# Performance work log

Measured on AMD Instinct MI355X. Metric: run time of the kernel, lower is better.

The kernel has to match this reference:

```python
import jax, jax.numpy as jnp
import numpy as np

N_NODES, N_EDGES, N_GRAPHS, D = 32768, 49152, 1024, 64


def setup_inputs() -> dict:
    key = jax.random.key(0)
    ks = jax.random.split(key, 24)
    p = lambda k, shape, s=0.1: jax.random.normal(k, shape, dtype=jnp.float32) * s
    return dict(
        x=jax.random.normal(ks[0], (N_NODES, 14), dtype=jnp.float32),
        edge_index=jax.random.randint(ks[1], (2, N_EDGES), 0, N_NODES),
        edge_attr=jax.random.uniform(ks[2], (N_EDGES, 4), dtype=jnp.float32),
        batch=jnp.sort(jax.random.randint(ks[3], (N_NODES,), 0, N_GRAPHS)),
        lin0_W=p(ks[4], (D, 14)), lin0_b=p(ks[5], (D,)),
        e1_W=p(ks[6], (128, 4)), e1_b=p(ks[7], (128,)),
        e2_W=p(ks[8], (D * D, 128), 0.02), e2_b=p(ks[9], (D * D,), 0.02),
        root_W=p(ks[10], (D, D)), conv_b=p(ks[11], (D,)),
        gru_Wih=p(ks[12], (3 * D, D)), gru_Whh=p(ks[13], (3 * D, D)),
        gru_bih=p(ks[14], (3 * D,)), gru_bhh=p(ks[15], (3 * D,)),
        lstm_Wih=p(ks[16], (4 * D, 2 * D)), lstm_Whh=p(ks[17], (4 * D, D)),
        lstm_bih=p(ks[18], (4 * D,)), lstm_bhh=p(ks[19], (4 * D,)),
        fc1_W=p(ks[20], (128, 2 * D)), fc1_b=p(ks[21], (128,)),
        fc2_W=p(ks[22], (1, 128)), fc2_b=p(ks[23], (1,)),
    )


def reference(x, edge_index, edge_attr, batch,
              lin0_W, lin0_b, e1_W, e1_b, e2_W, e2_b, root_W, conv_b,
              gru_Wih, gru_Whh, gru_bih, gru_bhh,
              lstm_Wih, lstm_Whh, lstm_bih, lstm_bhh,
              fc1_W, fc1_b, fc2_W, fc2_b):
    N, B = x.shape[0], N_GRAPHS
    src, dst = edge_index[0], edge_index[1]

    out = jax.nn.relu(x @ lin0_W.T + lin0_b)            # [N, D]
    h = out                                             # GRU hidden (num_layers=1)

    # Edge-conditioned weights: edge_attr is constant across the 3 iterations,
    # so compute the edge MLP once (identical math to re-running it).
    W = jax.nn.relu(edge_attr @ e1_W.T + e1_b) @ e2_W.T + e2_b
    W = W.reshape(-1, D, D)                             # [E, D, D]
    cnt = jnp.maximum(
        jax.ops.segment_sum(jnp.ones((src.shape[0],), x.dtype), dst, num_segments=N), 1.0)

    for _ in range(3):
        # NNConv (aggr='mean'): gather -> per-edge matmul -> scatter-mean -> root + bias
        msg = jnp.einsum('ei,eio->eo', out[src], W)     # [E, D]
        agg = jax.ops.segment_sum(msg, dst, num_segments=N) / cnt[:, None]
        m = jax.nn.relu(agg + out @ root_W + conv_b)
        # GRU cell (seq_len=1)
        gi = m @ gru_Wih.T + gru_bih
        gh = h @ gru_Whh.T + gru_bhh
        ir, iz, inn = jnp.split(gi, 3, -1)
        hr, hz, hn = jnp.split(gh, 3, -1)
        r = jax.nn.sigmoid(ir + hr)
        z = jax.nn.sigmoid(iz + hz)
        n = jnp.tanh(inn + r * hn)
        h = (1.0 - z) * n + z * h
        out = h

    # Set2Set pooling, 3 processing steps, LSTM(2D -> D)
    q_star = jnp.zeros((B, 2 * D), x.dtype)
    hl = jnp.zeros((B, D), x.dtype)
    cl = jnp.zeros((B, D), x.dtype)
    for _ in range(3):
        g = q_star @ lstm_Wih.T + lstm_bih + hl @ lstm_Whh.T + lstm_bhh
        i_, f_, g_, o_ = jnp.split(g, 4, -1)
        cl = jax.nn.sigmoid(f_) * cl + jax.nn.sigmoid(i_) * jnp.tanh(g_)
        hl = jax.nn.sigmoid(o_) * jnp.tanh(cl)
        q = hl                                          # [B, D]
        e = jnp.sum(out * q[batch], -1)                 # [N]
        mx = jax.ops.segment_max(e, batch, num_segments=B)
        ex = jnp.exp(e - mx[batch])
        den = jax.ops.segment_sum(ex, batch, num_segments=B)
        a = ex / den[batch]                             # segment softmax
        r_read = jax.ops.segment_sum(a[:, None] * out, batch, num_segments=B)
        q_star = jnp.concatenate([q, r_read], -1)       # [B, 2D]

    hid = jax.nn.relu(q_star @ fc1_W.T + fc1_b)
    return hid @ fc2_W.T + fc2_b                        # [B, 1]
```

## Files before the change

kernel.cpp:

```cpp
#include <hip/hip_runtime.h>
#include <math.h>

#define NN_ 32768
#define NE_ 49152
#define NG_ 1024

typedef short bh8 __attribute__((ext_vector_type(8)));
typedef float f32x4 __attribute__((ext_vector_type(4)));

__device__ __forceinline__ unsigned short f2bfu(float f) {
    union { float f; unsigned int i; } x; x.f = f;
    unsigned int u = x.i;
    u += 0x7FFFu + ((u >> 16) & 1u);
    return (unsigned short)(u >> 16);
}
__device__ __forceinline__ float sigm(float x) { return 1.f / (1.f + expf(-x)); }

__global__ void MPNN_78632261256134_kernel() {}

__global__ void k_zero(float* p, int n) {
    int i = blockIdx.x * 256 + threadIdx.x;
    if (i < n) p[i] = 0.f;
}

__global__ void k_init(float* cnt, float* qstar) {
    int i = blockIdx.x * 256 + threadIdx.x;
    if (i < NN_) cnt[i] = 0.f;
    else if (i < NN_ + NG_ * 256) qstar[i - NN_] = 0.f;
}

__global__ void k_lin0(const float* x, const float* W, const float* b, float* node) {
    int g = blockIdx.x * 256 + threadIdx.x;
    int n = g >> 6, d = g & 63;
    const float* xr = x + n * 14;
    const float* wr = W + d * 14;
    float acc = b[d];
    for (int i = 0; i < 14; i++) acc += xr[i] * wr[i];
    node[g] = fmaxf(acc, 0.f);
}

__global__ void k_cnt(const int* dst, float* cnt) {
    int e = blockIdx.x * 256 + threadIdx.x;
    if (e < NE_) atomicAdd(&cnt[dst[e]], 1.0f);
}

__global__ void k_tw(const float* gWih, const float* gWhh, float* WihT, float* WhhT,
                     const float* lWih, const float* lWhh, float* WihT2, float* WhhT2) {
    int t = blockIdx.x * 256 + threadIdx.x;
    if (t < 12288) {
        int gr = t >> 6, i = t & 63; WihT[i * 192 + gr] = gWih[t];
    } else if (t < 24576) {
        int u = t - 12288; int gr = u >> 6, i = u & 63; WhhT[i * 192 + gr] = gWhh[u];
    } else if (t < 57344) {
        int u = t - 24576; int r = u >> 7, c = u & 127; WihT2[c * 256 + r] = lWih[u];
    } else if (t < 73728) {
        int u = t - 57344; int r = u >> 6, c = u & 63; WhhT2[c * 256 + r] = lWhh[u];
    }
}

__global__ void k_bhat3(const float* e2W, unsigned short* Bhat3) {
    int idx = blockIdx.x * 256 + threadIdx.x;
    if (idx >= 64 * 4 * 4 * 64 * 8) return;
    int j = idx & 7, lane = (idx >> 3) & 63, t = (idx >> 9) & 3, w = (idx >> 11) & 3, s = idx >> 13;
    int row = s * 64 + w * 16 + (lane & 15);
    int k = t * 32 + (lane >> 4) * 8 + j;
    Bhat3[idx] = f2bfu(e2W[row * 128 + k]);
}

__global__ __launch_bounds__(256) void k_he(const float* __restrict__ ea,
                                            const float* __restrict__ e1W,
                                            const float* __restrict__ e1b,
                                            unsigned short* __restrict__ Hhat) {
    int tid = threadIdx.x;
    int lane = tid & 63, sub = tid >> 6;
    int gi = blockIdx.x * 4 + sub;
    int etile = gi >> 2, t = gi & 3;
    int e = etile * 16 + (lane & 15), quad = lane >> 4;
    const float* ar = ea + (size_t)e * 4;
    float a0 = ar[0], a1 = ar[1], a2 = ar[2], a3 = ar[3];
    union { unsigned short u[8]; uint4 q; } o;
#pragma unroll
    for (int j = 0; j < 8; j++) {
        int c = t * 32 + quad * 8 + j;
        const float* wr = e1W + c * 4;
        float h = e1b[c] + a0 * wr[0] + a1 * wr[1] + a2 * wr[2] + a3 * wr[3];
        o.u[j] = f2bfu(fmaxf(h, 0.f));
    }
    *(uint4*)(Hhat + (size_t)gi * 512 + lane * 8) = o.q;
}

#define PS(S) (((S) + soff) & 63)

#define LDB(B, S) {                                                                       \
        const unsigned short* _p = Bhat3 + (size_t)PS(S) * 8192 + w * 2048 + lane * 8;    \
        (B)[0] = *(const bh8*)(const void*)(_p);                                          \
        (B)[1] = *(const bh8*)(const void*)(_p + 512);                                    \
        (B)[2] = *(const bh8*)(const void*)(_p + 1024);                                   \
        (B)[3] = *(const bh8*)(const void*)(_p + 1536); }

#define MFMA16(ACC, B) {                                                                  \
        _Pragma("unroll")                                                                 \
        for (int t_ = 0; t_ < 4; t_++) {                                                  \
            _Pragma("unroll")                                                             \
            for (int mt_ = 0; mt_ < 4; mt_++)                                             \
                (ACC)[mt_] = __builtin_amdgcn_mfma_f32_16x16x32_bf16(                     \
                    af[mt_][t_], (B)[t_], (t_ == 0) ? z4 : (ACC)[mt_], 0, 0, 0);          \
        } }

#define CONSUME(ACC, S) {                                                                 \
        int sp_ = PS(S);                                                                  \
        float bb_ = ebs[sp_ * 64 + w * 16 + mrow];                                        \
        _Pragma("unroll")                                                                 \
        for (int mt_ = 0; mt_ < 4; mt_++) {                                               \
            f32x4 xv_ = *(const f32x4*)(const void*)(xs + sp_ * 68 + mt_ * 16 + quad * 4);\
            _Pragma("unroll")                                                             \
            for (int r_ = 0; r_ < 4; r_++)                                                \
                msg[mt_][r_] += xv_[r_] * ((ACC)[mt_][r_] + bb_);                         \
        } }

__global__ __launch_bounds__(256, 2) void k_convr(const float* __restrict__ node,
                                                  const unsigned short* __restrict__ Hhat,
                                                  const unsigned short* __restrict__ Bhat3,
                                                  const float* __restrict__ e2b,
                                                  const int* __restrict__ src,
                                                  const int* __restrict__ dst,
                                                  float* __restrict__ agg) {
    __shared__ __align__(16) float xs[64 * 68];
    __shared__ __align__(16) float ebs[64 * 64];
    __shared__ int dst_s[64];

    const int tid = threadIdx.x;
    const int eb = blockIdx.x * 64;
    const int lane = tid & 63, w = tid >> 6;
    const int quad = lane >> 4, mrow = lane & 15;
    const int soff = (blockIdx.x * 37) & 63;

    {
        int r = tid >> 2, c = tid & 3;
        int s = src[eb + r];
        const float* nr = node + (size_t)s * 64 + c * 16;
#pragma unroll
        for (int j = 0; j < 16; j++) xs[(c * 16 + j) * 68 + r] = nr[j];
#pragma unroll
        for (int j = 0; j < 16; j++) ebs[tid + 256 * j] = e2b[tid + 256 * j];
        if (tid < 64) dst_s[tid] = dst[eb + tid];
    }

    bh8 af[4][4];
#pragma unroll
    for (int mt = 0; mt < 4; mt++)
#pragma unroll
        for (int t = 0; t < 4; t++)
            af[mt][t] = *(const bh8*)(const void*)(
                Hhat + (size_t)(((eb >> 4) + mt) * 4 + t) * 512 + lane * 8);
    __syncthreads();

    const f32x4 z4 = {0.f, 0.f, 0.f, 0.f};
    f32x4 msg[4];
#pragma unroll
    for (int mt = 0; mt < 4; mt++) msg[mt] = z4;

    bh8 b0[4], b1[4];
    f32x4 accA[4], accB[4];

    LDB(b0, 0)
    LDB(b1, 1)
    MFMA16(accA, b0)
    LDB(b0, 2)

#pragma unroll 1
    for (int s = 0; s < 62; s += 2) {
        MFMA16(accB, b1)
        LDB(b1, s + 3)
        CONSUME(accA, s)
        MFMA16(accA, b0)
        LDB(b0, (s + 4) & 63)
        CONSUME(accB, s + 1)
    }
    MFMA16(accB, b1)
    CONSUME(accA, 62)
    CONSUME(accB, 63)

#pragma unroll
    for (int mt = 0; mt < 4; mt++)
#pragma unroll
        for (int r = 0; r < 4; r++)
            atomicAdd(agg + (size_t)dst_s[mt * 16 + quad * 4 + r] * 64 + w * 16 + mrow,
                      msg[mt][r]);
}

__global__ __launch_bounds__(256) void k_mgru(const float* __restrict__ agg,
                                              const float* __restrict__ cnt,
                                              const float* __restrict__ node,
                                              const float* __restrict__ rootW,
                                              const float* __restrict__ convb,
                                              const float* __restrict__ WihT,
                                              const float* __restrict__ WhhT,
                                              const float* __restrict__ bih,
                                              const float* __restrict__ bhh,
                                              float* __restrict__ hOut) {
    __shared__ __align__(16) float hsT[64][20];
    __shared__ __align__(16) float msT[64][20];
    const int tid = threadIdx.x;
    const int d = tid & 63, sub = tid >> 6;
    const int nb = blockIdx.x * 16;
    const int r0 = sub * 4;
    const int off = (blockIdx.x * 37) & 63;

    {
        f32x4 hv;
#pragma unroll
        for (int j = 0; j < 4; j++)
            hv[j] = node[(size_t)(nb + r0 + j) * 64 + d];
        *(f32x4*)&hsT[d][r0] = hv;
    }
    __syncthreads();

    {
        f32x4 root = {0.f, 0.f, 0.f, 0.f};
        for (int ii = 0; ii < 64; ii++) {
            int i = (ii + off) & 63;
            float wv = rootW[i * 64 + d];
            f32x4 h4 = *(const f32x4*)&hsT[i][r0];
#pragma unroll
            for (int j = 0; j < 4; j++) root[j] += h4[j] * wv;
        }
        float cb = convb[d];
        f32x4 mval;
#pragma unroll
        for (int j = 0; j < 4; j++) {
            int n = nb + r0 + j;
            float inv = 1.f / fmaxf(cnt[n], 1.f);
            mval[j] = fmaxf(agg[(size_t)n * 64 + d] * inv + cb + root[j], 0.f);
        }
        *(f32x4*)&msT[d][r0] = mval;
    }
    __syncthreads();

    float ir[4], iz[4], in_[4], hr[4], hz[4], hn[4];
    {
        float bi0 = bih[d], bi1 = bih[64 + d], bi2 = bih[128 + d];
        float bh0 = bhh[d], bh1 = bhh[64 + d], bh2 = bhh[128 + d];
#pragma unroll
        for (int j = 0; j < 4; j++) {
            ir[j] = bi0; iz[j] = bi1; in_[j] = bi2;
            hr[j] = bh0; hz[j] = bh1; hn[j] = bh2;
        }
    }
    for (int ii = 0; ii < 64; ii++) {
        int i = (ii + off) & 63;
        float wi0 = WihT[i * 192 + d];
        float wi1 = WihT[i * 192 + 64 + d];
        float wi2 = WihT[i * 192 + 128 + d];
        float wh0 = WhhT[i * 192 + d];
        float wh1 = WhhT[i * 192 + 64 + d];
        float wh2 = WhhT[i * 192 + 128 + d];
        f32x4 m4 = *(const f32x4*)&msT[i][r0];
        f32x4 h4 = *(const f32x4*)&hsT[i][r0];
#pragma unroll
        for (int j = 0; j < 4; j++) {
            ir[j] += m4[j] * wi0; iz[j] += m4[j] * wi1; in_[j] += m4[j] * wi2;
            hr[j] += h4[j] * wh0; hz[j] += h4[j] * wh1; hn[j] += h4[j] * wh2;
        }
    }
    f32x4 hold = *(const f32x4*)&hsT[d][r0];
#pragma unroll
    for (int j = 0; j < 4; j++) {
        float r = sigm(ir[j] + hr[j]);
        float z = sigm(iz[j] + hz[j]);
        float nn = tanhf(in_[j] + r * hn[j]);
        hOut[(size_t)(nb + r0 + j) * 64 + d] = (1.f - z) * nn + z * hold[j];
    }
}

__global__ __launch_bounds__(64) void k_s2s(const float* __restrict__ node,
                                            const int* __restrict__ batch,
                                            const float* __restrict__ WihT2,
                                            const float* __restrict__ WhhT2,
                                            const float* __restrict__ bih,
                                            const float* __restrict__ bhh,
                                            float* __restrict__ cl,
                                            float* __restrict__ hl,
                                            float* __restrict__ qstar) {
    __shared__ float qvs[128];
    __shared__ float hls[64];
    const int b = blockIdx.x, lane = threadIdx.x;
    const int joff = (b * 37) & 127;
    const int koff = (b * 37) & 63;

    qvs[lane] = qstar[(size_t)b * 128 + lane];
    qvs[64 + lane] = qstar[(size_t)b * 128 + 64 + lane];
    hls[lane] = hl[(size_t)b * 64 + lane];
    __syncthreads();

    float acc0 = bih[lane] + bhh[lane];
    float acc1 = bih[64 + lane] + bhh[64 + lane];
    float acc2 = bih[128 + lane] + bhh[128 + lane];
    float acc3 = bih[192 + lane] + bhh[192 + lane];
    for (int jj = 0; jj < 128; jj++) {
        int j = (jj + joff) & 127;
        float qj = qvs[j];
        const float* wr = WihT2 + (size_t)j * 256;
        acc0 += qj * wr[lane];
        acc1 += qj * wr[64 + lane];
        acc2 += qj * wr[128 + lane];
        acc3 += qj * wr[192 + lane];
    }
    for (int jj = 0; jj < 64; jj++) {
        int j = (jj + koff) & 63;
        float hj = hls[j];
        const float* wr = WhhT2 + (size_t)j * 256;
        acc0 += hj * wr[lane];
        acc1 += hj * wr[64 + lane];
        acc2 += hj * wr[128 + lane];
        acc3 += hj * wr[192 + lane];
    }
    float c = sigm(acc1) * cl[(size_t)b * 64 + lane] + sigm(acc0) * tanhf(acc2);
    cl[(size_t)b * 64 + lane] = c;
    float q = sigm(acc3) * tanhf(c);
    hl[(size_t)b * 64 + lane] = q;

    int lo = 0, hi = NN_;
    while (lo < hi) { int mid = (lo + hi) >> 1; if (batch[mid] < b) lo = mid + 1; else hi = mid; }
    int start = lo;
    lo = start; hi = NN_;
    while (lo < hi) { int mid = (lo + hi) >> 1; if (batch[mid] < b + 1) lo = mid + 1; else hi = mid; }
    int end = lo;

    float r_acc = 0.f, m_run = -1e30f, l_run = 0.f;
    for (int n = start; n < end; n++) {
        float nv = node[(size_t)n * 64 + lane];
        float p = nv * q;
#pragma unroll
        for (int o = 32; o > 0; o >>= 1) p += __shfl_xor(p, o);
        float m_new = fmaxf(m_run, p);
        float sc = expf(m_run - m_new);
        float wgt = expf(p - m_new);
        l_run = l_run * sc + wgt;
        r_acc = r_acc * sc + wgt * nv;
        m_run = m_new;
    }
    qstar[(size_t)b * 128 + lane] = q;
    qstar[(size_t)b * 128 + 64 + lane] = (end > start) ? r_acc / l_run : 0.f;
}

__global__ void k_fc(const float* qstar, const float* W1, const float* b1,
                     const float* W2, const float* b2, float* out) {
    __shared__ float hid[128];
    int b = blockIdx.x; int t = threadIdx.x;
    const float* qr = qstar + (size_t)b * 128;
    float acc = b1[t];
    const float* wr = W1 + (size_t)t * 128;
    for (int k = 0; k < 128; k++) acc += qr[k] * wr[k];
    hid[t] = fmaxf(acc, 0.f);
    __syncthreads();
    if (t < 64) {
        float s = hid[t] * W2[t] + hid[t + 64] * W2[t + 64];
        for (int o = 32; o > 0; o >>= 1) s += __shfl_xor(s, o);
        if (t == 0) out[b] = s + b2[0];
    }
}

extern "C" void kernel_launch(void* const* d_in, const int* in_sizes, int n_in,
                              void* d_out, int out_size, void* d_ws, size_t ws_size,
                              hipStream_t stream) {
    const float* x     = (const float*)d_in[0];
    const int*   ei    = (const int*)d_in[1];
    const float* ea    = (const float*)d_in[2];
    const int*   batch = (const int*)d_in[3];
    const float* lin0W = (const float*)d_in[4];
    const float* lin0b = (const float*)d_in[5];
    const float* e1W   = (const float*)d_in[6];
    const float* e1b   = (const float*)d_in[7];
    const float* e2W   = (const float*)d_in[8];
    const float* e2b   = (const float*)d_in[9];
    const float* rootW = (const float*)d_in[10];
    const float* convb = (const float*)d_in[11];
    const float* gWih  = (const float*)d_in[12];
    const float* gWhh  = (const float*)d_in[13];
    const float* gbih  = (const float*)d_in[14];
    const float* gbhh  = (const float*)d_in[15];
    const float* lWih  = (const float*)d_in[16];
    const float* lWhh  = (const float*)d_in[17];
    const float* lbih  = (const float*)d_in[18];
    const float* lbhh  = (const float*)d_in[19];
    const float* fc1W  = (const float*)d_in[20];
    const float* fc1b  = (const float*)d_in[21];
    const float* fc2W  = (const float*)d_in[22];
    const float* fc2b  = (const float*)d_in[23];
    const int* src = ei;
    const int* dst = ei + NE_;

    char* p = (char*)d_ws;
    auto alloc = [&](size_t bytes) -> char* {
        char* r = p; p += (bytes + 255) & ~(size_t)255; return r;
    };
    unsigned short* Bhat3 = (unsigned short*)alloc((size_t)524288 * 2);
    unsigned short* Hhat  = (unsigned short*)alloc((size_t)NE_ * 128 * 2);
    float* nodeA  = (float*)alloc((size_t)NN_ * 64 * 4);
    float* nodeB  = (float*)alloc((size_t)NN_ * 64 * 4);
    float* aggb   = (float*)alloc((size_t)NN_ * 64 * 4);
    float* cnt    = (float*)alloc((size_t)NN_ * 4);
    float* WihT   = (float*)alloc(192 * 64 * 4);
    float* WhhT   = (float*)alloc(192 * 64 * 4);
    float* WihT2  = (float*)alloc(256 * 128 * 4);
    float* WhhT2  = (float*)alloc(256 * 64 * 4);
    float* qstar  = (float*)alloc((size_t)NG_ * 128 * 4);
    float* hl     = (float*)alloc((size_t)NG_ * 64 * 4);
    float* clb    = (float*)alloc((size_t)NG_ * 64 * 4);

    k_init<<<(NN_ + NG_ * 256 + 255) / 256, 256, 0, stream>>>(cnt, qstar);
    k_lin0<<<NN_ * 64 / 256, 256, 0, stream>>>(x, lin0W, lin0b, nodeA);
    k_cnt<<<NE_ / 256, 256, 0, stream>>>(dst, cnt);
    k_tw<<<288, 256, 0, stream>>>(gWih, gWhh, WihT, WhhT, lWih, lWhh, WihT2, WhhT2);
    k_bhat3<<<524288 / 256, 256, 0, stream>>>(e2W, Bhat3);
    k_he<<<NE_ / 16, 256, 0, stream>>>(ea, e1W, e1b, Hhat);

    float* curF = nodeA; float* nxtF = nodeB;
    for (int it = 0; it < 3; it++) {
        k_zero<<<NN_ * 64 / 256, 256, 0, stream>>>(aggb, NN_ * 64);
        k_convr<<<NE_ / 64, 256, 0, stream>>>(curF, Hhat, Bhat3, e2b, src, dst, aggb);
        k_mgru<<<NN_ / 16, 256, 0, stream>>>(aggb, cnt, curF, rootW, convb,
                                             WihT, WhhT, gbih, gbhh, nxtF);
        float* tf = curF; curF = nxtF; nxtF = tf;
    }

    for (int s = 0; s < 3; s++)
        k_s2s<<<NG_, 64, 0, stream>>>(curF, batch, WihT2, WhhT2, lbih, lbhh, clb, hl, qstar);
    k_fc<<<NG_, 128, 0, stream>>>(qstar, fc1W, fc1b, fc2W, fc2b, (float*)d_out);
}
```

Baseline: 522.4 us.

## Fold agg zeroing into init and GRU, prefetch conv operands, raise MFMA priority

Drops the per-iteration k_zero launch. The aggregation buffer is now zeroed once in k_init, and k_mgru clears each entry after reading it, ready for the next iteration. In k_convr the per-block shared-memory copy of e2b is removed: bias values are read straight from global memory, and the node features and bias for the next step are loaded into registers one step ahead. The MFMA block is also wrapped in s_setprio so the matrix work gets issue priority. This saves three launches and a 64K-float LDS fill per block, at the cost of more registers in k_convr.

```diff
diff --git a/kernel.cpp b/kernel.cpp
--- a/kernel.cpp
+++ b/kernel.cpp
@@ -18,15 +18,13 @@
 
 __global__ void MPNN_78632261256134_kernel() {}
 
-__global__ void k_zero(float* p, int n) {
-    int i = blockIdx.x * 256 + threadIdx.x;
-    if (i < n) p[i] = 0.f;
-}
-
-__global__ void k_init(float* cnt, float* qstar) {
+__global__ void k_init(float* cnt, float* qstar, float* aggb) {
     int i = blockIdx.x * 256 + threadIdx.x;
     if (i < NN_) cnt[i] = 0.f;
-    else if (i < NN_ + NG_ * 256) qstar[i - NN_] = 0.f;
+    int j = i - NN_;
+    if (j >= 0 && j < NG_ * 256) qstar[j] = 0.f;
+    int k = i - NN_ - NG_ * 256;
+    if (k >= 0 && k < NN_ * 64) aggb[k] = 0.f;
 }
 
 __global__ void k_lin0(const float* x, const float* W, const float* b, float* node) {
@@ -98,24 +96,31 @@
         (B)[2] = *(const bh8*)(const void*)(_p + 1024);                                   \
         (B)[3] = *(const bh8*)(const void*)(_p + 1536); }
 
+#define LDXV(XV, S) {                                                                     \
+        int sp_ = PS(S);                                                                  \
+        _Pragma("unroll")                                                                 \
+        for (int mt_ = 0; mt_ < 4; mt_++)                                                 \
+            (XV)[mt_] = *(const f32x4*)(const void*)(xs + sp_ * 68 + mt_ * 16 + quad * 4); }
+
+#define LDBB(BB, S) (BB) = e2b[PS(S) * 64 + w * 16 + mrow];
+
 #define MFMA16(ACC, B) {                                                                  \
+        __builtin_amdgcn_s_setprio(1);                                                    \
         _Pragma("unroll")                                                                 \
         for (int t_ = 0; t_ < 4; t_++) {                                                  \
             _Pragma("unroll")                                                             \
             for (int mt_ = 0; mt_ < 4; mt_++)                                             \
                 (ACC)[mt_] = __builtin_amdgcn_mfma_f32_16x16x32_bf16(                     \
                     af[mt_][t_], (B)[t_], (t_ == 0) ? z4 : (ACC)[mt_], 0, 0, 0);          \
-        } }
-
-#define CONSUME(ACC, S) {                                                                 \
-        int sp_ = PS(S);                                                                  \
-        float bb_ = ebs[sp_ * 64 + w * 16 + mrow];                                        \
+        }                                                                                 \
+        __builtin_amdgcn_s_setprio(0); }
+
+#define CONSUME(ACC, XV, BB) {                                                            \
         _Pragma("unroll")                                                                 \
         for (int mt_ = 0; mt_ < 4; mt_++) {                                               \
-            f32x4 xv_ = *(const f32x4*)(const void*)(xs + sp_ * 68 + mt_ * 16 + quad * 4);\
             _Pragma("unroll")                                                             \
             for (int r_ = 0; r_ < 4; r_++)                                                \
-                msg[mt_][r_] += xv_[r_] * ((ACC)[mt_][r_] + bb_);                         \
+                msg[mt_][r_] += (XV)[mt_][r_] * ((ACC)[mt_][r_] + (BB));                  \
         } }
 
 __global__ __launch_bounds__(256, 2) void k_convr(const float* __restrict__ node,
@@ -126,7 +131,6 @@
                                                   const int* __restrict__ dst,
                                                   float* __restrict__ agg) {
     __shared__ __align__(16) float xs[64 * 68];
-    __shared__ __align__(16) float ebs[64 * 64];
     __shared__ int dst_s[64];
 
     const int tid = threadIdx.x;
@@ -141,8 +145,6 @@
         const float* nr = node + (size_t)s * 64 + c * 16;
 #pragma unroll
         for (int j = 0; j < 16; j++) xs[(c * 16 + j) * 68 + r] = nr[j];
-#pragma unroll
-        for (int j = 0; j < 16; j++) ebs[tid + 256 * j] = e2b[tid + 256 * j];
         if (tid < 64) dst_s[tid] = dst[eb + tid];
     }
 
@@ -161,10 +163,14 @@
     for (int mt = 0; mt < 4; mt++) msg[mt] = z4;
 
     bh8 b0[4], b1[4];
+    f32x4 xvA[4], xvB[4];
     f32x4 accA[4], accB[4];
+    float bbA, bbB;
 
     LDB(b0, 0)
     LDB(b1, 1)
+    LDXV(xvA, 0)
+    LDBB(bbA, 0)
     MFMA16(accA, b0)
     LDB(b0, 2)
 
@@ -172,14 +178,20 @@
     for (int s = 0; s < 62; s += 2) {
         MFMA16(accB, b1)
         LDB(b1, s + 3)
-        CONSUME(accA, s)
+        LDXV(xvB, s + 1)
+        LDBB(bbB, s + 1)
+        CONSUME(accA, xvA, bbA)
         MFMA16(accA, b0)
         LDB(b0, (s + 4) & 63)
-        CONSUME(accB, s + 1)
+        LDXV(xvA, s + 2)
+        LDBB(bbA, s + 2)
+        CONSUME(accB, xvB, bbB)
     }
     MFMA16(accB, b1)
-    CONSUME(accA, 62)
-    CONSUME(accB, 63)
+    CONSUME(accA, xvA, bbA)
+    LDXV(xvB, 63)
+    LDBB(bbB, 63)
+    CONSUME(accB, xvB, bbB)
 
 #pragma unroll
     for (int mt = 0; mt < 4; mt++)
@@ -189,7 +201,7 @@
                       msg[mt][r]);
 }
 
-__global__ __launch_bounds__(256) void k_mgru(const float* __restrict__ agg,
+__global__ __launch_bounds__(256) void k_mgru(float* __restrict__ agg,
                                               const float* __restrict__ cnt,
                                               const float* __restrict__ node,
                                               const float* __restrict__ rootW,
@@ -231,7 +243,9 @@
         for (int j = 0; j < 4; j++) {
             int n = nb + r0 + j;
             float inv = 1.f / fmaxf(cnt[n], 1.f);
-            mval[j] = fmaxf(agg[(size_t)n * 64 + d] * inv + cb + root[j], 0.f);
+            float av = agg[(size_t)n * 64 + d];
+            agg[(size_t)n * 64 + d] = 0.f;
+            mval[j] = fmaxf(av * inv + cb + root[j], 0.f);
         }
         *(f32x4*)&msT[d][r0] = mval;
     }
@@ -409,7 +423,7 @@
     float* hl     = (float*)alloc((size_t)NG_ * 64 * 4);
     float* clb    = (float*)alloc((size_t)NG_ * 64 * 4);
 
-    k_init<<<(NN_ + NG_ * 256 + 255) / 256, 256, 0, stream>>>(cnt, qstar);
+    k_init<<<(NN_ + NG_ * 256 + NN_ * 64 + 255) / 256, 256, 0, stream>>>(cnt, qstar, aggb);
     k_lin0<<<NN_ * 64 / 256, 256, 0, stream>>>(x, lin0W, lin0b, nodeA);
     k_cnt<<<NE_ / 256, 256, 0, stream>>>(dst, cnt);
     k_tw<<<288, 256, 0, stream>>>(gWih, gWhh, WihT, WhhT, lWih, lWhh, WihT2, WhhT2);
@@ -418,7 +432,6 @@
 
     float* curF = nodeA; float* nxtF = nodeB;
     for (int it = 0; it < 3; it++) {
-        k_zero<<<NN_ * 64 / 256, 256, 0, stream>>>(aggb, NN_ * 64);
         k_convr<<<NE_ / 64, 256, 0, stream>>>(curF, Hhat, Bhat3, e2b, src, dst, aggb);
         k_mgru<<<NN_ / 16, 256, 0, stream>>>(aggb, cnt, curF, rootW, convb,
                                              WihT, WhhT, gbih, gbhh, nxtF);
```

Result: no change. 514.8 us (-1.5%).
